# Performance work log

Measured on AMD Instinct MI355X. Metric: run time of the kernel, lower is better.

The kernel has to match this reference:

```python
import jax, jax.numpy as jnp
import numpy as np

N = 50000      # nodes
E = 800000     # edges (before self-loops)
IN = 128       # input_dim
H = 4          # heads in conv1
C = 128        # per-head channels
G = 128        # num graphs in batch
OUT = 8        # output_dim
EPS = 1e-5


def layer_norm(x, g, b):
    mu = jnp.mean(x, axis=-1, keepdims=True)
    var = jnp.var(x, axis=-1, keepdims=True)
    return (x - mu) * jax.lax.rsqrt(var + EPS) * g + b


def gat_conv(x, src, dst, W, att_src, att_dst, bias, heads, ch):
    n = x.shape[0]
    h = (x @ W).reshape(n, heads, ch)                      # [N,H,C]
    a_src = jnp.einsum('nhc,hc->nh', h, att_src)           # [N,H]
    a_dst = jnp.einsum('nhc,hc->nh', h, att_dst)
    e = jax.nn.leaky_relu(a_src[src] + a_dst[dst], 0.2)    # [E,H]
    e_max = jax.ops.segment_max(e, dst, num_segments=n)
    e_max = jnp.where(jnp.isfinite(e_max), e_max, 0.0)
    ex = jnp.exp(e - e_max[dst])
    denom = jax.ops.segment_sum(ex, dst, num_segments=n)
    alpha = ex / (denom[dst] + 1e-16)                      # segment softmax over dst
    msg = h[src] * alpha[:, :, None]                       # [E,H,C]
    out = jax.ops.segment_sum(msg, dst, num_segments=n)    # [N,H,C]
    return out.reshape(n, heads * ch) + bias


def _forward(x, edge_index, batch, params):
    (W1, as1, ad1, b1, g1, be1, W2, as2, ad2, b2, g2, be2,
     rW1, rb1, rg, rbe, rW2, rb2) = params
    # add self-loops (PyG GATConv default)
    loop = jnp.arange(N)
    src = jnp.concatenate([edge_index[0], loop])
    dst = jnp.concatenate([edge_index[1], loop])
    h1 = jax.nn.relu(layer_norm(gat_conv(x, src, dst, W1, as1, ad1, b1, H, C), g1, be1))
    h2 = jax.nn.relu(layer_norm(gat_conv(h1, src, dst, W2, as2, ad2, b2, 1, C), g2, be2))
    # global mean pool
    sums = jax.ops.segment_sum(h2, batch, num_segments=G)
    cnt = jax.ops.segment_sum(jnp.ones((N, 1), h2.dtype), batch, num_segments=G)
    pooled = sums / jnp.maximum(cnt, 1.0)
    r = jax.nn.relu(layer_norm(pooled @ rW1 + rb1, rg, rbe))
    return r @ rW2 + rb2                                   # [G, OUT]


def setup_inputs() -> dict:
    key = jax.random.key(0)
    ks = jax.random.split(key, 24)
    s = 0.05
    return {
        'x': jax.random.normal(ks[0], (N, IN), jnp.float32),
        'edge_index': jax.random.randint(ks[1], (2, E), 0, N),
        'edge_weight': jax.random.uniform(ks[2], (E,), jnp.float32),
        'batch': jnp.sort(jax.random.randint(ks[3], (N,), 0, G)),
        'W1': jax.random.normal(ks[4], (IN, H * C), jnp.float32) * s,
        'att_src1': jax.random.normal(ks[5], (H, C), jnp.float32) * s,
        'att_dst1': jax.random.normal(ks[6], (H, C), jnp.float32) * s,
        'b1': jnp.zeros((H * C,), jnp.float32),
        'g1': jnp.ones((H * C,), jnp.float32),
        'be1': jnp.zeros((H * C,), jnp.float32),
        'W2': jax.random.normal(ks[7], (H * C, C), jnp.float32) * s,
        'att_src2': jax.random.normal(ks[8], (1, C), jnp.float32) * s,
        'att_dst2': jax.random.normal(ks[9], (1, C), jnp.float32) * s,
        'b2': jnp.zeros((C,), jnp.float32),
        'g2': jnp.ones((C,), jnp.float32),
        'be2': jnp.zeros((C,), jnp.float32),
        'rW1': jax.random.normal(ks[10], (C, 32), jnp.float32) * s,
        'rb1': jnp.zeros((32,), jnp.float32),
        'rg': jnp.ones((32,), jnp.float32),
        'rbe': jnp.zeros((32,), jnp.float32),
        'rW2': jax.random.normal(ks[11], (32, OUT), jnp.float32) * s,
        'rb2': jnp.zeros((OUT,), jnp.float32),
    }


def reference(x, edge_index, edge_weight, batch, W1, att_src1, att_dst1, b1, g1, be1,
              W2, att_src2, att_dst2, b2, g2, be2, rW1, rb1, rg, rbe, rW2, rb2):
    # edge_weight is accepted but unused, matching the original forward
    params = (W1, att_src1, att_dst1, b1, g1, be1, W2, att_src2, att_dst2, b2, g2, be2,
              rW1, rb1, rg, rbe, rW2, rb2)
    return _forward(x, edge_index, batch, params)
```

## Files before the change

### kernel.cpp

```cpp
#include <hip/hip_runtime.h>
#include <math.h>

#define HEADS 4
#define CH 128
#define HC 512
#define GRAPHS 128
#define OUT_DIM 8

typedef unsigned short u16;
typedef unsigned int u32;
typedef short short8 __attribute__((ext_vector_type(8)));
typedef float f32x4 __attribute__((ext_vector_type(4)));
typedef float f32x2 __attribute__((ext_vector_type(2)));

__device__ inline u16 f2b(float f) {
  u32 u = __float_as_uint(f);
  u32 r = u + 0x7FFFu + ((u >> 16) & 1u);
  return (u16)(r >> 16);
}
__device__ inline float blo(u32 d) { return __uint_as_float(d << 16); }
__device__ inline float bhi(u32 d) { return __uint_as_float(d & 0xffff0000u); }
__device__ inline f32x2 bunpack(u32 d) {
  f32x2 r; r.x = blo(d); r.y = bhi(d); return r;
}
__device__ inline float lrelu(float v) { return v > 0.f ? v : 0.2f * v; }
__device__ inline int rdl(int v, int l) { return __builtin_amdgcn_readlane(v, l); }
__device__ inline float rdlf(float v, int l) {
  return __int_as_float(__builtin_amdgcn_readlane(__float_as_int(v), l));
}

__global__ __launch_bounds__(256) void k_scanA(const int* __restrict__ counts,
                                               int* __restrict__ bsum, int N) {
  __shared__ int sh[256];
  int b = blockIdx.x, t = threadIdx.x, i = b * 256 + t;
  sh[t] = (i < N) ? counts[i] : 0;
  __syncthreads();
  for (int off = 128; off; off >>= 1) {
    if (t < off) sh[t] += sh[t + off];
    __syncthreads();
  }
  if (t == 0) bsum[b] = sh[0];
}

__global__ __launch_bounds__(1024) void k_scanB(const int* __restrict__ bsum,
                                                int* __restrict__ boff, int nb) {
  __shared__ int sh[1024];
  int t = threadIdx.x;
  sh[t] = (t < nb) ? bsum[t] : 0;
  __syncthreads();
  for (int off = 1; off < 1024; off <<= 1) {
    int v = sh[t];
    int u = (t >= off) ? sh[t - off] : 0;
    __syncthreads();
    sh[t] = v + u;
    __syncthreads();
  }
  if (t < nb) boff[t] = (t == 0) ? 0 : sh[t - 1];
}

__global__ __launch_bounds__(256) void k_scanC(const int* __restrict__ counts,
                                               const int* __restrict__ boff,
                                               int* __restrict__ indptr,
                                               int* __restrict__ cursor, int N) {
  __shared__ int sh[256];
  int b = blockIdx.x, t = threadIdx.x, i = b * 256 + t;
  int v = (i < N) ? counts[i] : 0;
  sh[t] = v;
  __syncthreads();
  for (int off = 1; off < 256; off <<= 1) {
    int a = sh[t];
    int u = (t >= off) ? sh[t - off] : 0;
    __syncthreads();
    sh[t] = a + u;
    __syncthreads();
  }
  if (i < N) {
    int excl = boff[b] + sh[t] - v;
    indptr[i] = excl;
    cursor[i] = excl;
    if (i == N - 1) indptr[N] = excl + v;
  }
}

__global__ void k_scatter(const int* __restrict__ ei, int* __restrict__ cursor,
                          int* __restrict__ srcs, int E, int N) {
  int total = E + N;
  int base = blockIdx.x * 1024 + threadIdx.x;
  #pragma unroll
  for (int u = 0; u < 4; u++) {
    int i = base + u * 256;
    if (i < total) {
      int src, dst;
      if (i < E) { src = ei[i]; dst = ei[E + i]; } else { src = i - E; dst = i - E; }
      int pos = atomicAdd(&cursor[dst], 1);
      srcs[pos] = src;
    }
  }
}

__global__ __launch_bounds__(256) void k_wprep(const float* __restrict__ W1,
                                               const float* __restrict__ W2,
                                               const float* __restrict__ as1,
                                               const float* __restrict__ ad1,
                                               u16* __restrict__ W1t,
                                               u16* __restrict__ W2t,
                                               u16* __restrict__ wst) {
  int b = blockIdx.x, t = threadIdx.x;
  if (b < 256) {
    int i = b * 256 + t;
    int n = i >> 7, k = i & 127;
    W1t[i] = f2b(W1[(size_t)k * HC + n]);
  } else if (b < 512) {
    int i = (b - 256) * 256 + t;
    int n = i >> 9, k = i & 511;
    W2t[i] = f2b(W2[(size_t)k * CH + n]);
  } else {
    for (int idx = t; idx < 16 * 128; idx += 256) {
      int o = idx >> 7, k = idx & 127;
      float s = 0.f;
      if (o < 8) {
        int h = o & 3;
        const float* av = ((o < 4) ? as1 : ad1) + h * CH;
        const float* wrow = W1 + (size_t)k * HC + h * CH;
        for (int c = 0; c < CH; c++) s += wrow[c] * av[c];
      }
      wst[idx] = f2b(s);
    }
  }
}

__global__ void k_count_prep(const int* __restrict__ ei, int* __restrict__ counts,
                             int E, int N, int eb,
                             const float* __restrict__ x, uint2* __restrict__ xb2) {
  if ((int)blockIdx.x < eb) {
    int total = E + N;
    int base = blockIdx.x * 1024 + threadIdx.x;
    #pragma unroll
    for (int u = 0; u < 4; u++) {
      int i = base + u * 256;
      if (i < total) {
        int dst = (i < E) ? ei[E + i] : (i - E);
        atomicAdd(&counts[dst], 1);
      }
    }
    return;
  }
  int i = (blockIdx.x - eb) * 256 + threadIdx.x;
  if (i >= N * 32) return;
  float4 v = ((const float4*)x)[i];
  uint2 o;
  o.x = (u32)f2b(v.x) | ((u32)f2b(v.y) << 16);
  o.y = (u32)f2b(v.z) | ((u32)f2b(v.w) << 16);
  xb2[i] = o;
}

__global__ __launch_bounds__(256) void k_score(
    const u16* __restrict__ xb, const u16* __restrict__ wst,
    float* __restrict__ sa1, float* __restrict__ da1, int N) {
  int lane = threadIdx.x & 63, wid = threadIdx.x >> 6;
  int base = (blockIdx.x * 4 + wid) * 64;
  if (base >= N) return;
  int lr = lane & 15, lk = lane >> 4;
  short8 bfrag[4];
  #pragma unroll
  for (int ks = 0; ks < 4; ks++)
    bfrag[ks] = *(const short8*)(wst + lr * 128 + ks * 32 + lk * 8);
  #pragma unroll
  for (int rt = 0; rt < 4; rt++) {
    int r0 = base + rt * 16;
    if (r0 >= N) break;
    f32x4 acc = {};
    int row = r0 + lr; if (row >= N) row = N - 1;
    #pragma unroll
    for (int ks = 0; ks < 4; ks++) {
      short8 afrag = *(const short8*)(xb + (size_t)row * 128 + ks * 32 + lk * 8);
      acc = __builtin_amdgcn_mfma_f32_16x16x32_bf16(afrag, bfrag[ks], acc, 0, 0, 0);
    }
    int col = lr;
    #pragma unroll
    for (int r = 0; r < 4; r++) {
      int n = r0 + lk * 4 + r;
      if (n < N) {
        if (col < 4) sa1[n * 4 + col] = acc[r];
        else if (col < 8) da1[n * 4 + (col - 4)] = acc[r];
      }
    }
  }
}

__global__ __launch_bounds__(256) void k_aggx(
    const u32* __restrict__ xb, const int* __restrict__ indptr,
    const int* __restrict__ srcs, const float4* __restrict__ as1,
    const float4* __restrict__ ad1, u32* __restrict__ aggx, int N) {
  __shared__ __align__(16) float s_w0[4][64][4];
  __shared__ __align__(16) float s_w1[4][64][4];
  int t = threadIdx.x;
  int lane = t & 63, wid = t >> 6;
  int n0 = blockIdx.x * 8 + wid * 2;
  if (n0 >= N) return;
  int n1 = n0 + 1;
  bool has1 = n1 < N;
  int beg0 = indptr[n0], end0 = indptr[n0 + 1];
  int beg1 = end0, end1 = has1 ? indptr[n1 + 1] : end0;
  int deg0 = end0 - beg0, deg1 = end1 - beg1;
  float4 ad0 = ad1[n0];
  float4 adv1 = has1 ? ad1[n1] : make_float4(0.f, 0.f, 0.f, 0.f);

  if (deg0 <= 64 && deg1 <= 64) {
    int s0 = 0, s1 = 0;
    float w0[4] = {}, w1[4] = {};
    if (lane < deg0) {
      s0 = srcs[beg0 + lane];
      float4 a = as1[s0];
      w0[0] = __expf(lrelu(a.x + ad0.x)); w0[1] = __expf(lrelu(a.y + ad0.y));
      w0[2] = __expf(lrelu(a.z + ad0.z)); w0[3] = __expf(lrelu(a.w + ad0.w));
    }
    if (lane < deg1) {
      s1 = srcs[beg1 + lane];
      float4 a = as1[s1];
      w1[0] = __expf(lrelu(a.x + adv1.x)); w1[1] = __expf(lrelu(a.y + adv1.y));
      w1[2] = __expf(lrelu(a.z + adv1.z)); w1[3] = __expf(lrelu(a.w + adv1.w));
    }
    *(float4*)&s_w0[wid][lane][0] = make_float4(w0[0], w0[1], w0[2], w0[3]);
    *(float4*)&s_w1[wid][lane][0] = make_float4(w1[0], w1[1], w1[2], w1[3]);
    f32x2 c0[4] = {}, c1[4] = {};
    int dboth = (deg0 < deg1 ? deg0 : deg1) & ~3;
    int j = 0;
    for (; j < dboth; j += 4) {
      u32 d[4], e[4];
      #pragma unroll
      for (int u = 0; u < 4; u++) d[u] = xb[(size_t)rdl(s0, j + u) * 64 + lane];
      #pragma unroll
      for (int u = 0; u < 4; u++) e[u] = xb[(size_t)rdl(s1, j + u) * 64 + lane];
      #pragma unroll
      for (int u = 0; u < 4; u++) {
        f32x2 xv = bunpack(d[u]);
        f32x2 yv = bunpack(e[u]);
        float4 wv0 = *(const float4*)&s_w0[wid][j + u][0];
        float4 wv1 = *(const float4*)&s_w1[wid][j + u][0];
        c0[0] += xv * wv0.x; c0[1] += xv * wv0.y; c0[2] += xv * wv0.z; c0[3] += xv * wv0.w;
        c1[0] += yv * wv1.x; c1[1] += yv * wv1.y; c1[2] += yv * wv1.z; c1[3] += yv * wv1.w;
      }
    }
    int pad0 = (deg0 + 3) & ~3;
    for (int ja = j; ja < pad0; ja += 4) {
      u32 d[4];
      #pragma unroll
      for (int u = 0; u < 4; u++) d[u] = xb[(size_t)rdl(s0, ja + u) * 64 + lane];
      #pragma unroll
      for (int u = 0; u < 4; u++) {
        f32x2 xv = bunpack(d[u]);
        float4 wv0 = *(const float4*)&s_w0[wid][ja + u][0];
        c0[0] += xv * wv0.x; c0[1] += xv * wv0.y; c0[2] += xv * wv0.z; c0[3] += xv * wv0.w;
      }
    }
    int pad1 = (deg1 + 3) & ~3;
    for (int jb = j; jb < pad1; jb += 4) {
      u32 e[4];
      #pragma unroll
      for (int u = 0; u < 4; u++) e[u] = xb[(size_t)rdl(s1, jb + u) * 64 + lane];
      #pragma unroll
      for (int u = 0; u < 4; u++) {
        f32x2 yv = bunpack(e[u]);
        float4 wv1 = *(const float4*)&s_w1[wid][jb + u][0];
        c1[0] += yv * wv1.x; c1[1] += yv * wv1.y; c1[2] += yv * wv1.z; c1[3] += yv * wv1.w;
      }
    }
    float e0[4], e1[4];
    #pragma unroll
    for (int h = 0; h < 4; h++) {
      float v0 = w0[h], v1 = w1[h];
      #pragma unroll
      for (int off = 32; off; off >>= 1) {
        v0 += __shfl_xor(v0, off);
        v1 += __shfl_xor(v1, off);
      }
      e0[h] = v0; e1[h] = v1;
    }
    {
      u32* orow = aggx + (size_t)n0 * 256;
      #pragma unroll
      for (int h = 0; h < 4; h++) {
        float iv = 1.f / (e0[h] + 1e-16f);
        orow[h * 64 + lane] = (u32)f2b(c0[h].x * iv) | ((u32)f2b(c0[h].y * iv) << 16);
      }
    }
    if (has1) {
      u32* orow = aggx + (size_t)n1 * 256;
      #pragma unroll
      for (int h = 0; h < 4; h++) {
        float iv = 1.f / (e1[h] + 1e-16f);
        orow[h * 64 + lane] = (u32)f2b(c1[h].x * iv) | ((u32)f2b(c1[h].y * iv) << 16);
      }
    }
    return;
  }
  for (int pass = 0; pass < 2; pass++) {
    if (pass == 1 && !has1) break;
    int n = pass ? n1 : n0;
    int beg = pass ? beg1 : beg0;
    int end = pass ? end1 : end0;
    float4 ad = pass ? adv1 : ad0;
    float e0[4] = {};
    f32x2 c0[4] = {};
    for (int base = beg; base < end; base += 64) {
      int cnt = min(64, end - base);
      int sreg = 0;
      float w0[4] = {};
      if (lane < cnt) {
        sreg = srcs[base + lane];
        float4 a = as1[sreg];
        w0[0] = __expf(lrelu(a.x + ad.x)); w0[1] = __expf(lrelu(a.y + ad.y));
        w0[2] = __expf(lrelu(a.z + ad.z)); w0[3] = __expf(lrelu(a.w + ad.w));
      }
      int cpad = (cnt + 1) & ~1;
      for (int j = 0; j < cpad; j += 2) {
        u32 dA = xb[(size_t)rdl(sreg, j) * 64 + lane];
        u32 dB = xb[(size_t)rdl(sreg, j + 1) * 64 + lane];
        f32x2 xA = bunpack(dA), xB = bunpack(dB);
        #pragma unroll
        for (int h = 0; h < 4; h++) {
          float a = rdlf(w0[h], j), b = rdlf(w0[h], j + 1);
          e0[h] += a + b;
          c0[h] += xA * a;
          c0[h] += xB * b;
        }
      }
    }
    u32* orow = aggx + (size_t)n * 256;
    #pragma unroll
    for (int h = 0; h < 4; h++) {
      float iv = 1.f / (e0[h] + 1e-16f);
      orow[h * 64 + lane] = (u32)f2b(c0[h].x * iv) | ((u32)f2b(c0[h].y * iv) << 16);
    }
  }
}

__global__ __launch_bounds__(256) void k_gemm_head(
    const u16* __restrict__ A,
    const u16* __restrict__ Bt,
    const float* __restrict__ bias,
    u16* __restrict__ C,
    int M) {
  __shared__ u16 As[128 * 64];
  __shared__ u16 Bs[128 * 64];
  int t = threadIdx.x;
  int lane = t & 63, wid = t >> 6;
  int wr = wid >> 1, wc = wid & 1;
  int r0 = blockIdx.x * 128;
  int hh = blockIdx.y;
  const u16* Ah = A + hh * 128;
  const u16* Bh = Bt + (size_t)hh * 128 * 128;
  int lr = lane & 15, lk = lane >> 4;
  f32x4 acc[4][4] = {};
  for (int kt = 0; kt < 128; kt += 64) {
    #pragma unroll
    for (int it = 0; it < 4; it++) {
      int q = wid * 4096 + it * 1024 + lane * 16;
      int row = q >> 7;
      int soff = ((q >> 4) & 7) ^ (row & 7);
      {
        int gr = r0 + row; if (gr >= M) gr = M - 1;
        const u16* gp = Ah + (size_t)gr * 512 + kt + soff * 8;
        __builtin_amdgcn_global_load_lds(
            (const __attribute__((address_space(1))) void*)gp,
            (__attribute__((address_space(3))) void*)((char*)As + wid * 4096 + it * 1024),
            16, 0, 0);
      }
      {
        const u16* gp = Bh + (size_t)row * 128 + kt + soff * 8;
        __builtin_amdgcn_global_load_lds(
            (const __attribute__((address_space(1))) void*)gp,
            (__attribute__((address_space(3))) void*)((char*)Bs + wid * 4096 + it * 1024),
            16, 0, 0);
      }
    }
    __syncthreads();
    const char* Ab = (const char*)As;
    const char* Bb = (const char*)Bs;
    #pragma unroll
    for (int kk = 0; kk < 2; kk++) {
      short8 a[4], b[4];
      #pragma unroll
      for (int m = 0; m < 4; m++) {
        int row = wr * 64 + m * 16 + lr;
        int off = (row << 7) + kk * 64 + lk * 16;
        off ^= (row & 7) << 4;
        a[m] = *(const short8*)(Ab + off);
      }
      #pragma unroll
      for (int nn = 0; nn < 4; nn++) {
        int row = wc * 64 + nn * 16 + lr;
        int off = (row << 7) + kk * 64 + lk * 16;
        off ^= (row & 7) << 4;
        b[nn] = *(const short8*)(Bb + off);
      }
      #pragma unroll
      for (int m = 0; m < 4; m++)
        #pragma unroll
        for (int nn = 0; nn < 4; nn++)
          acc[m][nn] = __builtin_amdgcn_mfma_f32_16x16x32_bf16(a[m], b[nn], acc[m][nn], 0, 0, 0);
    }
    __syncthreads();
  }
  #pragma unroll
  for (int m = 0; m < 4; m++)
    #pragma unroll
    for (int nn = 0; nn < 4; nn++)
      #pragma unroll
      for (int r = 0; r < 4; r++) {
        int row = r0 + wr * 64 + m * 16 + lk * 4 + r;
        if (row < M) {
          int gcol = hh * 128 + wc * 64 + nn * 16 + lr;
          C[(size_t)row * 512 + gcol] = f2b(acc[m][nn][r] + bias[gcol]);
        }
      }
}

__global__ __launch_bounds__(256) void k_ln512(const u16* __restrict__ raw,
                                               const float* __restrict__ gam,
                                               const float* __restrict__ bet,
                                               u16* __restrict__ out, int N) {
  int n = blockIdx.x * 4 + (threadIdx.x >> 6);
  int lane = threadIdx.x & 63;
  if (n >= N) return;
  const uint4* r = (const uint4*)(raw + (size_t)n * 512);
  uint4 q = r[lane];
  float v[8];
  v[0] = blo(q.x); v[1] = bhi(q.x); v[2] = blo(q.y); v[3] = bhi(q.y);
  v[4] = blo(q.z); v[5] = bhi(q.z); v[6] = blo(q.w); v[7] = bhi(q.w);
  float s1 = 0.f, s2 = 0.f;
  #pragma unroll
  for (int j = 0; j < 8; j++) { s1 += v[j]; s2 += v[j] * v[j]; }
  #pragma unroll
  for (int off = 32; off; off >>= 1) {
    s1 += __shfl_xor(s1, off);
    s2 += __shfl_xor(s2, off);
  }
  float mean = s1 * (1.f / 512.f);
  float var = s2 * (1.f / 512.f) - mean * mean;
  float rs = rsqrtf(var + 1e-5f);
  u32 o[4];
  #pragma unroll
  for (int j = 0; j < 4; j++) {
    int ch = lane * 8 + 2 * j;
    float y0 = fmaxf((v[2 * j] - mean) * rs * gam[ch] + bet[ch], 0.f);
    float y1 = fmaxf((v[2 * j + 1] - mean) * rs * gam[ch + 1] + bet[ch + 1], 0.f);
    o[j] = (u32)f2b(y0) | ((u32)f2b(y1) << 16);
  }
  ((uint4*)(out + (size_t)n * 512))[lane] = make_uint4(o[0], o[1], o[2], o[3]);
}

__global__ __launch_bounds__(256) void k_gemm_bf16(
    const u16* __restrict__ A, const u16* __restrict__ Bt,
    u16* __restrict__ C, int M, int Nc, int K) {
  __shared__ u16 As[128 * 64];
  __shared__ u16 Bs[128 * 64];
  int t = threadIdx.x;
  int lane = t & 63, wid = t >> 6;
  int wr = wid >> 1, wc = wid & 1;
  int r0 = blockIdx.x * 128, c0 = blockIdx.y * 128;
  int lr = lane & 15, lk = lane >> 4;
  f32x4 acc[4][4] = {};
  for (int kt = 0; kt < K; kt += 64) {
    #pragma unroll
    for (int it = 0; it < 4; it++) {
      int q = wid * 4096 + it * 1024 + lane * 16;
      int row = q >> 7;
      int soff = ((q >> 4) & 7) ^ (row & 7);
      {
        int gr = r0 + row; if (gr >= M) gr = M - 1;
        const u16* gp = A + (size_t)gr * K + kt + soff * 8;
        __builtin_amdgcn_global_load_lds(
            (const __attribute__((address_space(1))) void*)gp,
            (__attribute__((address_space(3))) void*)((char*)As + wid * 4096 + it * 1024),
            16, 0, 0);
      }
      {
        int gn = c0 + row;
        const u16* gp = Bt + (size_t)gn * K + kt + soff * 8;
        __builtin_amdgcn_global_load_lds(
            (const __attribute__((address_space(1))) void*)gp,
            (__attribute__((address_space(3))) void*)((char*)Bs + wid * 4096 + it * 1024),
            16, 0, 0);
      }
    }
    __syncthreads();
    const char* Ab = (const char*)As;
    const char* Bb = (const char*)Bs;
    #pragma unroll
    for (int kk = 0; kk < 2; kk++) {
      short8 a[4], b[4];
      #pragma unroll
      for (int m = 0; m < 4; m++) {
        int row = wr * 64 + m * 16 + lr;
        int off = (row << 7) + kk * 64 + lk * 16;
        off ^= (row & 7) << 4;
        a[m] = *(const short8*)(Ab + off);
      }
      #pragma unroll
      for (int nn = 0; nn < 4; nn++) {
        int row = wc * 64 + nn * 16 + lr;
        int off = (row << 7) + kk * 64 + lk * 16;
        off ^= (row & 7) << 4;
        b[nn] = *(const short8*)(Bb + off);
      }
      #pragma unroll
      for (int m = 0; m < 4; m++)
        #pragma unroll
        for (int nn = 0; nn < 4; nn++)
          acc[m][nn] = __builtin_amdgcn_mfma_f32_16x16x32_bf16(a[m], b[nn], acc[m][nn], 0, 0, 0);
    }
    __syncthreads();
  }
  #pragma unroll
  for (int m = 0; m < 4; m++)
    #pragma unroll
    for (int nn = 0; nn < 4; nn++)
      #pragma unroll
      for (int r = 0; r < 4; r++) {
        int row = r0 + wr * 64 + m * 16 + lk * 4 + r;
        if (row < M) {
          int col = c0 + wc * 64 + nn * 16 + lr;
          C[(size_t)row * Nc + col] = f2b(acc[m][nn][r]);
        }
      }
}

__global__ void k_att_h1(const u16* __restrict__ hm, const float* __restrict__ att_s,
                         const float* __restrict__ att_d, float* __restrict__ s_out,
                         float* __restrict__ d_out, int N) {
  int n = blockIdx.x * (blockDim.x >> 6) + (threadIdx.x >> 6);
  int lane = threadIdx.x & 63;
  if (n >= N) return;
  const u32* row = (const u32*)(hm + (size_t)n * CH);
  u32 d = row[lane];
  float x0 = blo(d), x1 = bhi(d);
  float ps = x0 * att_s[2 * lane] + x1 * att_s[2 * lane + 1];
  float pd = x0 * att_d[2 * lane] + x1 * att_d[2 * lane + 1];
  #pragma unroll
  for (int off = 32; off; off >>= 1) {
    ps += __shfl_xor(ps, off);
    pd += __shfl_xor(pd, off);
  }
  if (lane == 0) { s_out[n] = ps; d_out[n] = pd; }
}

__global__ __launch_bounds__(256) void k_agg2f(
    const u32* __restrict__ raw2, const int* __restrict__ indptr,
    const int* __restrict__ srcs, const float* __restrict__ as2,
    const float* __restrict__ ad2, const float* __restrict__ bias,
    const float* __restrict__ gam, const float* __restrict__ bet,
    float* __restrict__ h2, int N) {
  int t = threadIdx.x;
  int lane = t & 63, wid = t >> 6;
  int n0 = blockIdx.x * 8 + wid * 2;
  if (n0 >= N) return;
  int n1 = n0 + 1;
  bool has1 = n1 < N;
  int beg0 = indptr[n0], end0 = indptr[n0 + 1];
  int beg1 = end0, end1 = has1 ? indptr[n1 + 1] : end0;
  int deg0 = end0 - beg0, deg1 = end1 - beg1;
  float adv0 = ad2[n0];
  float adv1 = has1 ? ad2[n1] : 0.f;
  float ds0 = 0.f, ds1 = 0.f;
  f32x2 acc0 = {0.f, 0.f}, acc1 = {0.f, 0.f};

  if (deg0 <= 64 && deg1 <= 64) {
    int s0 = 0, s1r = 0;
    float w0 = 0.f, w1 = 0.f;
    if (lane < deg0) { s0 = srcs[beg0 + lane]; w0 = __expf(lrelu(as2[s0] + adv0)); }
    if (lane < deg1) { s1r = srcs[beg1 + lane]; w1 = __expf(lrelu(as2[s1r] + adv1)); }
    int dboth = (deg0 < deg1 ? deg0 : deg1) & ~7;
    int j = 0;
    for (; j < dboth; j += 8) {
      u32 d[8], e[8];
      #pragma unroll
      for (int u = 0; u < 8; u++) d[u] = raw2[(size_t)rdl(s0, j + u) * 64 + lane];
      #pragma unroll
      for (int u = 0; u < 8; u++) e[u] = raw2[(size_t)rdl(s1r, j + u) * 64 + lane];
      #pragma unroll
      for (int u = 0; u < 8; u++) {
        acc0 += bunpack(d[u]) * rdlf(w0, j + u);
        acc1 += bunpack(e[u]) * rdlf(w1, j + u);
      }
    }
    int pad0 = (deg0 + 3) & ~3;
    for (int ja = j; ja < pad0; ja += 4) {
      u32 d[4];
      #pragma unroll
      for (int u = 0; u < 4; u++) d[u] = raw2[(size_t)rdl(s0, ja + u) * 64 + lane];
      #pragma unroll
      for (int u = 0; u < 4; u++) acc0 += bunpack(d[u]) * rdlf(w0, ja + u);
    }
    int pad1 = (deg1 + 3) & ~3;
    for (int jb = j; jb < pad1; jb += 4) {
      u32 e[4];
      #pragma unroll
      for (int u = 0; u < 4; u++) e[u] = raw2[(size_t)rdl(s1r, jb + u) * 64 + lane];
      #pragma unroll
      for (int u = 0; u < 4; u++) acc1 += bunpack(e[u]) * rdlf(w1, jb + u);
    }
    float v0 = w0, v1 = w1;
    #pragma unroll
    for (int off = 32; off; off >>= 1) {
      v0 += __shfl_xor(v0, off);
      v1 += __shfl_xor(v1, off);
    }
    ds0 = v0; ds1 = v1;
  } else {
    for (int pass = 0; pass < 2; pass++) {
      if (pass == 1 && !has1) break;
      int beg = pass ? beg1 : beg0;
      int end = pass ? end1 : end0;
      float adv = pass ? adv1 : adv0;
      for (int base = beg; base < end; base += 64) {
        int cnt = min(64, end - base);
        int sreg = 0;
        float w = 0.f;
        if (lane < cnt) { sreg = srcs[base + lane]; w = __expf(lrelu(as2[sreg] + adv)); }
        int cpad = (cnt + 3) & ~3;
        for (int j = 0; j < cpad; j += 4) {
          u32 dA = raw2[(size_t)rdl(sreg, j) * 64 + lane];
          u32 dB = raw2[(size_t)rdl(sreg, j + 1) * 64 + lane];
          u32 dC = raw2[(size_t)rdl(sreg, j + 2) * 64 + lane];
          u32 dD = raw2[(size_t)rdl(sreg, j + 3) * 64 + lane];
          float wA = rdlf(w, j), wB = rdlf(w, j + 1);
          float wC = rdlf(w, j + 2), wD = rdlf(w, j + 3);
          f32x2 s = bunpack(dA) * wA;
          s += bunpack(dB) * wB;
          s += bunpack(dC) * wC;
          s += bunpack(dD) * wD;
          float sw = (wA + wB) + (wC + wD);
          if (pass) { ds1 += sw; acc1 += s; }
          else      { ds0 += sw; acc0 += s; }
        }
      }
    }
  }

  float inv0 = 1.f / (ds0 + 1e-16f);
  float v00 = acc0.x * inv0 + bias[2 * lane];
  float v01 = acc0.y * inv0 + bias[2 * lane + 1];
  float s1a = v00 + v01, s2a = v00 * v00 + v01 * v01;
  float inv1 = 1.f / (ds1 + 1e-16f);
  float v10 = acc1.x * inv1 + bias[2 * lane];
  float v11 = acc1.y * inv1 + bias[2 * lane + 1];
  float s1b = v10 + v11, s2b = v10 * v10 + v11 * v11;
  #pragma unroll
  for (int off = 32; off; off >>= 1) {
    s1a += __shfl_xor(s1a, off);
    s2a += __shfl_xor(s2a, off);
    s1b += __shfl_xor(s1b, off);
    s2b += __shfl_xor(s2b, off);
  }
  {
    float mean = s1a * (1.f / 128.f);
    float var = s2a * (1.f / 128.f) - mean * mean;
    float rs = rsqrtf(var + 1e-5f);
    float y0 = fmaxf((v00 - mean) * rs * gam[2 * lane] + bet[2 * lane], 0.f);
    float y1 = fmaxf((v01 - mean) * rs * gam[2 * lane + 1] + bet[2 * lane + 1], 0.f);
    ((float2*)(h2 + (size_t)n0 * 128))[lane] = make_float2(y0, y1);
  }
  if (has1) {
    float mean = s1b * (1.f / 128.f);
    float var = s2b * (1.f / 128.f) - mean * mean;
    float rs = rsqrtf(var + 1e-5f);
    float y0 = fmaxf((v10 - mean) * rs * gam[2 * lane] + bet[2 * lane], 0.f);
    float y1 = fmaxf((v11 - mean) * rs * gam[2 * lane + 1] + bet[2 * lane + 1], 0.f);
    ((float2*)(h2 + (size_t)n1 * 128))[lane] = make_float2(y0, y1);
  }
}

__global__ __launch_bounds__(256) void k_head(const float* __restrict__ h2,
    const int* __restrict__ batch, int N,
    const float* __restrict__ rW1, const float* __restrict__ rb1,
    const float* __restrict__ rg, const float* __restrict__ rbe,
    const float* __restrict__ rW2, const float* __restrict__ rb2,
    float* __restrict__ outp) {
  int g = blockIdx.x, t = threadIdx.x;
  int ch = t & 127, half = t >> 7;
  __shared__ float part[2][128];
  __shared__ float pl[128];
  __shared__ float yv[32];
  __shared__ float rv[32];
  __shared__ float mv[2];
  __shared__ int sseg[2];
  if (t == 0) {
    int lo = 0, hi = N;
    while (lo < hi) { int mid = (lo + hi) >> 1; if (batch[mid] < g) lo = mid + 1; else hi = mid; }
    int lo2 = lo, hi2 = N;
    while (lo2 < hi2) { int mid = (lo2 + hi2) >> 1; if (batch[mid] < g + 1) lo2 = mid + 1; else hi2 = mid; }
    sseg[0] = lo; sseg[1] = lo2;
  }
  __syncthreads();
  int lo = sseg[0], hi = sseg[1];
  float s = 0.f;
  int n = lo + half;
  for (; n + 8 <= hi; n += 8) {
    s += h2[(size_t)n * 128 + ch] + h2[(size_t)(n + 2) * 128 + ch]
       + h2[(size_t)(n + 4) * 128 + ch] + h2[(size_t)(n + 6) * 128 + ch];
  }
  for (; n < hi; n += 2) s += h2[(size_t)n * 128 + ch];
  part[half][ch] = s;
  __syncthreads();
  float cnt = fmaxf((float)(hi - lo), 1.f);
  if (t < 128) pl[t] = (part[0][t] + part[1][t]) / cnt;
  __syncthreads();
  if (t < 32) {
    float sum = rb1[t];
    for (int c = 0; c < 128; c++) sum += pl[c] * rW1[c * 32 + t];
    yv[t] = sum;
  }
  __syncthreads();
  if (t == 0) {
    float sm = 0.f, sq = 0.f;
    for (int j = 0; j < 32; j++) { sm += yv[j]; sq += yv[j] * yv[j]; }
    float mean = sm / 32.f;
    float var = sq / 32.f - mean * mean;
    mv[0] = mean; mv[1] = rsqrtf(var + 1e-5f);
  }
  __syncthreads();
  if (t < 32) {
    float y = (yv[t] - mv[0]) * mv[1] * rg[t] + rbe[t];
    rv[t] = fmaxf(y, 0.f);
  }
  __syncthreads();
  if (t < OUT_DIM) {
    float sum = rb2[t];
    for (int j = 0; j < 32; j++) sum += rv[j] * rW2[j * 8 + t];
    outp[g * 8 + t] = sum;
  }
}

extern "C" void kernel_launch(void* const* d_in, const int* in_sizes, int n_in,
                              void* d_out, int out_size, void* d_ws, size_t ws_size,
                              hipStream_t stream) {
  const float* x    = (const float*)d_in[0];
  const int*   ei   = (const int*)d_in[1];
  const int*   batch= (const int*)d_in[3];
  const float* W1   = (const float*)d_in[4];
  const float* as1w = (const float*)d_in[5];
  const float* ad1w = (const float*)d_in[6];
  const float* b1   = (const float*)d_in[7];
  const float* g1   = (const float*)d_in[8];
  const float* be1  = (const float*)d_in[9];
  const float* W2   = (const float*)d_in[10];
  const float* as2w = (const float*)d_in[11];
  const float* ad2w = (const float*)d_in[12];
  const float* b2   = (const float*)d_in[13];
  const float* g2   = (const float*)d_in[14];
  const float* be2  = (const float*)d_in[15];
  const float* rW1  = (const float*)d_in[16];
  const float* rb1  = (const float*)d_in[17];
  const float* rg   = (const float*)d_in[18];
  const float* rbe  = (const float*)d_in[19];
  const float* rW2  = (const float*)d_in[20];
  const float* rb2  = (const float*)d_in[21];

  int N = in_sizes[0] / 128;
  int E = in_sizes[1] / 2;
  int ET = E + N;
  int nb = (N + 255) / 256;

  char* p = (char*)d_ws;
  u16* x_b   = (u16*)p; p += (size_t)N * 128 * 2;
  u16* aggx  = (u16*)p; p += (size_t)N * 512 * 2;
  u16* raw1  = (u16*)p; p += (size_t)N * 512 * 2;
  u16* h1_b  = (u16*)p; p += (size_t)N * 512 * 2;
  u16* raw2b = (u16*)p; p += (size_t)N * 128 * 2;
  float* h2  = (float*)p; p += (size_t)N * 128 * 4;
  u16* W1t   = (u16*)p; p += 512 * 128 * 2;
  u16* W2t   = (u16*)p; p += 128 * 512 * 2;
  u16* wst   = (u16*)p; p += 16 * 128 * 2;
  float* sa1 = (float*)p; p += (size_t)N * 4 * 4;
  float* da1 = (float*)p; p += (size_t)N * 4 * 4;
  float* sa2 = (float*)p; p += (size_t)N * 4;
  float* da2 = (float*)p; p += (size_t)N * 4;
  int* counts = (int*)p; p += (size_t)N * 4;
  int* indptr = (int*)p; p += (size_t)(N + 1) * 4;
  int* cursor = (int*)p; p += (size_t)N * 4;
  int* bsum   = (int*)p; p += (size_t)nb * 4;
  int* boff   = (int*)p; p += (size_t)nb * 4;
  int* srcs   = (int*)p; p += (size_t)ET * 4;

  hipMemsetAsync(counts, 0, (size_t)N * sizeof(int), stream);

  int eb4 = (ET + 1023) / 1024;

  k_wprep<<<513, 256, 0, stream>>>(W1, W2, as1w, ad1w, W1t, W2t, wst);

  int cb = (N * 32 + 255) / 256;
  k_count_prep<<<eb4 + cb, 256, 0, stream>>>(ei, counts, E, N, eb4, x, (uint2*)x_b);

  k_score<<<(N + 255) / 256, 256, 0, stream>>>(x_b, wst, sa1, da1, N);

  k_scanA<<<nb, 256, 0, stream>>>(counts, bsum, N);
  k_scanB<<<1, 1024, 0, stream>>>(bsum, boff, nb);
  k_scanC<<<nb, 256, 0, stream>>>(counts, boff, indptr, cursor, N);
  k_scatter<<<eb4, 256, 0, stream>>>(ei, cursor, srcs, E, N);

  k_aggx<<<(N + 7) / 8, 256, 0, stream>>>((const u32*)x_b, indptr, srcs,
                                          (const float4*)sa1, (const float4*)da1,
                                          (u32*)aggx, N);
  dim3 gridh((N + 127) / 128, 4);
  k_gemm_head<<<gridh, 256, 0, stream>>>(aggx, W1t, b1, raw1, N);
  k_ln512<<<(N + 3) / 4, 256, 0, stream>>>(raw1, g1, be1, h1_b, N);

  dim3 grid2((N + 127) / 128, 1);
  k_gemm_bf16<<<grid2, 256, 0, stream>>>(h1_b, W2t, raw2b, N, 128, 512);
  k_att_h1<<<(N + 3) / 4, 256, 0, stream>>>(raw2b, as2w, ad2w, sa2, da2, N);
  k_agg2f<<<(N + 7) / 8, 256, 0, stream>>>((const u32*)raw2b, indptr, srcs, sa2, da2,
                                           b2, g2, be2, h2, N);

  k_head<<<GRAPHS, 256, 0, stream>>>(h2, batch, N, rW1, rb1, rg, rbe, rW2, rb2,
                                     (float*)d_out);
}
```

Baseline: 326.1 us.

## Replace atomic CSR scatter with bucketed two-pass counting sort

Builds the destination-sorted source list with a two-level counting sort instead of global atomic cursors. Edge chunks record per-bucket histograms, a column scan assigns chunk offsets, pairs are placed into node buckets, and a per-bucket kernel finishes placement with shared-memory cursors. The aim is to cut contended random global atomics and scattered writes. In exchange it adds two kernels, a serial single-block scan and an extra pass over 8-byte pairs.

```diff
diff --git a/kernel.cpp b/kernel.cpp
--- a/kernel.cpp
+++ b/kernel.cpp
@@ -6,6 +6,7 @@
 #define HC 512
 #define GRAPHS 128
 #define OUT_DIM 8
+#define PCHUNK 4096
 
 typedef unsigned short u16;
 typedef unsigned int u32;
@@ -60,8 +61,7 @@
 
 __global__ __launch_bounds__(256) void k_scanC(const int* __restrict__ counts,
                                                const int* __restrict__ boff,
-                                               int* __restrict__ indptr,
-                                               int* __restrict__ cursor, int N) {
+                                               int* __restrict__ indptr, int N) {
   __shared__ int sh[256];
   int b = blockIdx.x, t = threadIdx.x, i = b * 256 + t;
   int v = (i < N) ? counts[i] : 0;
@@ -77,24 +77,7 @@
   if (i < N) {
     int excl = boff[b] + sh[t] - v;
     indptr[i] = excl;
-    cursor[i] = excl;
     if (i == N - 1) indptr[N] = excl + v;
-  }
-}
-
-__global__ void k_scatter(const int* __restrict__ ei, int* __restrict__ cursor,
-                          int* __restrict__ srcs, int E, int N) {
-  int total = E + N;
-  int base = blockIdx.x * 1024 + threadIdx.x;
-  #pragma unroll
-  for (int u = 0; u < 4; u++) {
-    int i = base + u * 256;
-    if (i < total) {
-      int src, dst;
-      if (i < E) { src = ei[i]; dst = ei[E + i]; } else { src = i - E; dst = i - E; }
-      int pos = atomicAdd(&cursor[dst], 1);
-      srcs[pos] = src;
-    }
   }
 }
 
@@ -129,29 +112,101 @@
   }
 }
 
-__global__ void k_count_prep(const int* __restrict__ ei, int* __restrict__ counts,
-                             int E, int N, int eb,
-                             const float* __restrict__ x, uint2* __restrict__ xb2) {
-  if ((int)blockIdx.x < eb) {
+__global__ __launch_bounds__(256) void k_count_prep(
+    const int* __restrict__ ei, int* __restrict__ counts,
+    int* __restrict__ blockhist, int E, int N, int PB,
+    const float* __restrict__ x, uint2* __restrict__ xb2) {
+  int t = threadIdx.x;
+  if ((int)blockIdx.x < PB) {
+    __shared__ int hist[256];
+    hist[t] = 0;
+    __syncthreads();
     int total = E + N;
-    int base = blockIdx.x * 1024 + threadIdx.x;
-    #pragma unroll
-    for (int u = 0; u < 4; u++) {
-      int i = base + u * 256;
+    int base = blockIdx.x * PCHUNK;
+    #pragma unroll 4
+    for (int u = 0; u < 16; u++) {
+      int i = base + u * 256 + t;
       if (i < total) {
-        int dst = (i < E) ? ei[E + i] : (i - E);
-        atomicAdd(&counts[dst], 1);
-      }
-    }
+        int d = (i < E) ? ei[E + i] : (i - E);
+        atomicAdd(&counts[d], 1);
+        atomicAdd(&hist[d >> 8], 1);
+      }
+    }
+    __syncthreads();
+    blockhist[blockIdx.x * 256 + t] = hist[t];
     return;
   }
-  int i = (blockIdx.x - eb) * 256 + threadIdx.x;
+  int i = ((int)blockIdx.x - PB) * 256 + t;
   if (i >= N * 32) return;
   float4 v = ((const float4*)x)[i];
   uint2 o;
   o.x = (u32)f2b(v.x) | ((u32)f2b(v.y) << 16);
   o.y = (u32)f2b(v.z) | ((u32)f2b(v.w) << 16);
   xb2[i] = o;
+}
+
+__global__ __launch_bounds__(256) void k_colscan(const int* __restrict__ blockhist,
+                                                 const int* __restrict__ indptr,
+                                                 int* __restrict__ gbase, int N, int PB) {
+  int b = threadIdx.x;
+  int nb0 = b << 8; if (nb0 > N) nb0 = N;
+  int run = indptr[nb0];
+  #pragma unroll 8
+  for (int p = 0; p < PB; p++) {
+    int h = blockhist[p * 256 + b];
+    gbase[p * 256 + b] = run;
+    run += h;
+  }
+}
+
+__global__ __launch_bounds__(256) void k_place(const int* __restrict__ ei,
+                                               const int* __restrict__ gbase,
+                                               uint2* __restrict__ bpairs,
+                                               int E, int N) {
+  __shared__ int hist[256];
+  int t = threadIdx.x;
+  hist[t] = 0;
+  __syncthreads();
+  int total = E + N;
+  int base = blockIdx.x * PCHUNK;
+  int lrank[16];
+  #pragma unroll 4
+  for (int u = 0; u < 16; u++) {
+    int i = base + u * 256 + t;
+    lrank[u] = -1;
+    if (i < total) {
+      int d = (i < E) ? ei[E + i] : (i - E);
+      lrank[u] = atomicAdd(&hist[d >> 8], 1);
+    }
+  }
+  const int* gb = gbase + blockIdx.x * 256;
+  #pragma unroll 4
+  for (int u = 0; u < 16; u++) {
+    if (lrank[u] >= 0) {
+      int i = base + u * 256 + t;
+      int s, d;
+      if (i < E) { s = ei[i]; d = ei[E + i]; } else { s = i - E; d = i - E; }
+      bpairs[gb[d >> 8] + lrank[u]] = make_uint2((u32)s, (u32)d);
+    }
+  }
+}
+
+__global__ __launch_bounds__(256) void k_scatter2(const uint2* __restrict__ bpairs,
+                                                  const int* __restrict__ indptr,
+                                                  int* __restrict__ srcs, int N) {
+  __shared__ int curs[256];
+  int b = blockIdx.x, t = threadIdx.x;
+  int nbeg = b << 8;
+  int nend = nbeg + 256; if (nend > N) nend = N;
+  int ebeg = indptr[nbeg], eend = indptr[nend];
+  curs[t] = 0;
+  __syncthreads();
+  for (int i = ebeg + t; i < eend; i += 256) {
+    uint2 p = bpairs[i];
+    int d = (int)p.y;
+    int r = atomicAdd(&curs[d - nbeg], 1);
+    srcs[indptr[d] + r] = (int)p.x;
+  }
 }
 
 __global__ __launch_bounds__(256) void k_score(
@@ -337,11 +392,8 @@
 }
 
 __global__ __launch_bounds__(256) void k_gemm_head(
-    const u16* __restrict__ A,
-    const u16* __restrict__ Bt,
-    const float* __restrict__ bias,
-    u16* __restrict__ C,
-    int M) {
+    const u16* __restrict__ A, const u16* __restrict__ Bt,
+    const float* __restrict__ bias, u16* __restrict__ C, int M) {
   __shared__ u16 As[128 * 64];
   __shared__ u16 Bs[128 * 64];
   int t = threadIdx.x;
@@ -762,6 +814,8 @@
   int E = in_sizes[1] / 2;
   int ET = E + N;
   int nb = (N + 255) / 256;
+  int PB = (ET + PCHUNK - 1) / PCHUNK;
+  int nbk = (N + 255) >> 8;
 
   char* p = (char*)d_ws;
   u16* x_b   = (u16*)p; p += (size_t)N * 128 * 2;
@@ -779,26 +833,30 @@
   float* da2 = (float*)p; p += (size_t)N * 4;
   int* counts = (int*)p; p += (size_t)N * 4;
   int* indptr = (int*)p; p += (size_t)(N + 1) * 4;
-  int* cursor = (int*)p; p += (size_t)N * 4;
   int* bsum   = (int*)p; p += (size_t)nb * 4;
   int* boff   = (int*)p; p += (size_t)nb * 4;
+  int* blockhist = (int*)p; p += (size_t)PB * 256 * 4;
+  int* gbase  = (int*)p; p += (size_t)PB * 256 * 4;
   int* srcs   = (int*)p; p += (size_t)ET * 4;
+  uint2* bpairs = (uint2*)p; p += (size_t)ET * 8;
 
   hipMemsetAsync(counts, 0, (size_t)N * sizeof(int), stream);
 
-  int eb4 = (ET + 1023) / 1024;
-
   k_wprep<<<513, 256, 0, stream>>>(W1, W2, as1w, ad1w, W1t, W2t, wst);
 
   int cb = (N * 32 + 255) / 256;
-  k_count_prep<<<eb4 + cb, 256, 0, stream>>>(ei, counts, E, N, eb4, x, (uint2*)x_b);
+  k_count_prep<<<PB + cb, 256, 0, stream>>>(ei, counts, blockhist, E, N, PB,
+                                            x, (uint2*)x_b);
 
   k_score<<<(N + 255) / 256, 256, 0, stream>>>(x_b, wst, sa1, da1, N);
 
   k_scanA<<<nb, 256, 0, stream>>>(counts, bsum, N);
   k_scanB<<<1, 1024, 0, stream>>>(bsum, boff, nb);
-  k_scanC<<<nb, 256, 0, stream>>>(counts, boff, indptr, cursor, N);
-  k_scatter<<<eb4, 256, 0, stream>>>(ei, cursor, srcs, E, N);
+  k_scanC<<<nb, 256, 0, stream>>>(counts, boff, indptr, N);
+
+  k_colscan<<<1, 256, 0, stream>>>(blockhist, indptr, gbase, N, PB);
+  k_place<<<PB, 256, 0, stream>>>(ei, gbase, bpairs, E, N);
+  k_scatter2<<<nbk, 256, 0, stream>>>(bpairs, indptr, srcs, N);
 
   k_aggx<<<(N + 7) / 8, 256, 0, stream>>>((const u32*)x_b, indptr, srcs,
                                           (const float4*)sa1, (const float4*)da1,
```

After: 306.7 us. 1.06x faster.
